# Optimization experiments

Measured on AMD Instinct MI355X. Metric: run time of the kernel, lower is better.

## Reference

```python
import jax, jax.numpy as jnp
import numpy as np

B, L, H, C = 2, 512, 128, 25

def setup_inputs() -> dict:
    key = jax.random.key(0)
    k1, k2, k3, k4 = jax.random.split(key, 4)
    x1 = jax.random.normal(k1, (B, L, H), dtype=jnp.float32)
    x2 = jax.random.normal(k2, (B, L, H), dtype=jnp.float32)
    W = jax.random.normal(k3, (C, 4 * H), dtype=jnp.float32) * (1.0 / np.sqrt(4 * H))
    b = jax.random.normal(k4, (C,), dtype=jnp.float32) * 0.01
    return {"x1": x1, "x2": x2, "W": W, "b": b}

def reference(x1, x2, W, b):
    # feat = cat([x1_i, x2_j, x1_i*x2_j, |x1_i - x2_j|]) over all (i, j) pairs,
    # then Linear(4H -> C). Split W into its 4 H-sized blocks so we never
    # materialize the [B, L, L, 4H] concatenated tensor.
    Hd = x1.shape[-1]
    W1, W2, W3, W4 = (W[:, 0:Hd], W[:, Hd:2*Hd], W[:, 2*Hd:3*Hd], W[:, 3*Hd:4*Hd])
    a = x1[:, :, None, :]   # [B, L, 1, H] -> row token
    c = x2[:, None, :, :]   # [B, 1, L, H] -> col token
    # a@W1 and c@W2 depend on only one index, so compute [B, L, C] then broadcast.
    t1 = jnp.einsum('blh,ch->blc', x1, W1)[:, :, None, :]  # [B, L, 1, C]
    t2 = jnp.einsum('blh,ch->blc', x2, W2)[:, None, :, :]  # [B, 1, L, C]
    # product term is a bilinear contraction; no [B,L,L,H] materialization needed.
    t3 = jnp.einsum('blh,bmh,ch->blmc', x1, x2, W3)         # [B, L, L, C]
    # abs-diff term requires the pairwise [B, L, L, H] tensor (nonlinear in pair).
    t4 = jnp.einsum('blmh,ch->blmc', jnp.abs(a - c), W4)    # [B, L, L, C]
    return t1 + t2 + t3 + t4 + b  # [B, L, L, C]
```

## Files before the change

kernel.cpp:

```cpp
#include <hip/hip_runtime.h>
#include <hip/hip_bf16.h>
#include <math.h>

#define BB 2
#define LL 512
#define HH 128
#define CC 25
#define W4H (4*HH)

typedef __attribute__((ext_vector_type(4))) float    f32x4;
typedef __attribute__((ext_vector_type(8))) _Float16 half8;
typedef __attribute__((ext_vector_type(2))) _Float16 half2t;
typedef __attribute__((ext_vector_type(4))) unsigned uint4v;

#define MTILE 64
#define LPB   8
#define XPH   136

static __device__ __forceinline__ half8 habs8(half8 x) {
    uint4v u = __builtin_bit_cast(uint4v, x);
    u &= 0x7FFF7FFFu;
    return __builtin_bit_cast(half8, u);
}
static __device__ __forceinline__ half2t pkrtz(float a, float b) {
    return __builtin_bit_cast(half2t, __builtin_amdgcn_cvt_pkrtz(a, b));
}
union H4 { half2t h2[2]; unsigned long long u64; };
union H8 { half2t h2[4]; uint4v u4; half8 h8; };

static __device__ __forceinline__ half8 loadWfrag(const float* __restrict__ W,
                                                  int c, int col0) {
    H8 h; h.u4 = (uint4v){0u, 0u, 0u, 0u};
    if (c < CC) {
        const float* p = W + (size_t)c * W4H + col0;
        const f32x4 v0 = *(const f32x4*)(p);
        const f32x4 v1 = *(const f32x4*)(p + 4);
        h.h2[0] = pkrtz(v0[0], v0[1]);
        h.h2[1] = pkrtz(v0[2], v0[3]);
        h.h2[2] = pkrtz(v1[0], v1[1]);
        h.h2[3] = pkrtz(v1[2], v1[3]);
    }
    return h.h8;
}

__global__ __launch_bounds__(256)
void biaffine_fused(const float* __restrict__ x1, const float* __restrict__ x2,
                    const float* __restrict__ W, const float* __restrict__ bias,
                    float* __restrict__ out)
{
    __shared__ __align__(16) _Float16 x1h[LPB * XPH];
    __shared__ __align__(16) float    t1s[LPB * 32];

    const int tid = threadIdx.x;
    const int b   = blockIdx.z;
    const int l0  = blockIdx.y * LPB;
    const int m0  = blockIdx.x * MTILE;

    const int lane = tid & 63;
    const int wv   = tid >> 6;
    const int q    = lane >> 4;
    const int cn   = lane & 15;

    {
        const float* sx1 = x1 + ((size_t)b * LL + l0) * HH;
        const int r  = tid >> 5;
        const int c4 = tid & 31;
        const f32x4 v = *(const f32x4*)(sx1 + r * HH + c4 * 4);
        H4 h;
        h.h2[0] = pkrtz(v[0], v[1]);
        h.h2[1] = pkrtz(v[2], v[3]);
        *(unsigned long long*)(&x1h[r * XPH + c4 * 4]) = h.u64;
    }
    __syncthreads();

    const int mrowA = wv * 16 + cn;
    half8 X2f[4];
    {
        const float* px2 = x2 + ((size_t)b * LL + m0 + mrowA) * HH;
        #pragma unroll
        for (int hh = 0; hh < 4; ++hh) {
            const float* p = px2 + hh * 32 + q * 8;
            const f32x4 v0 = *(const f32x4*)(p);
            const f32x4 v1 = *(const f32x4*)(p + 4);
            H8 h;
            h.h2[0] = pkrtz(v0[0], v0[1]);
            h.h2[1] = pkrtz(v0[2], v0[3]);
            h.h2[2] = pkrtz(v1[0], v1[1]);
            h.h2[3] = pkrtz(v1[2], v1[3]);
            X2f[hh] = h.h8;
        }
    }

    f32x4 t2a = {0.f,0.f,0.f,0.f}, t2b = {0.f,0.f,0.f,0.f};
    #pragma unroll
    for (int kk = 0; kk < 4; ++kk) {
        const int col0 = HH + kk * 32 + q * 8;
        const half8 b0 = loadWfrag(W, cn,      col0);
        const half8 b1 = loadWfrag(W, cn + 16, col0);
        t2a = __builtin_amdgcn_mfma_f32_16x16x32_f16(X2f[kk], b0, t2a, 0, 0, 0);
        t2b = __builtin_amdgcn_mfma_f32_16x16x32_f16(X2f[kk], b1, t2b, 0, 0, 0);
    }

    if (wv == 0) {
        f32x4 t1acc0 = {0.f,0.f,0.f,0.f}, t1acc1 = {0.f,0.f,0.f,0.f};
        #pragma unroll
        for (int kk = 0; kk < 4; ++kk) {
            const half8 a1 = *(const half8*)(&x1h[(cn & 7) * XPH + kk * 32 + q * 8]);
            const int col0 = kk * 32 + q * 8;
            const half8 b0 = loadWfrag(W, cn,      col0);
            const half8 b1 = loadWfrag(W, cn + 16, col0);
            t1acc0 = __builtin_amdgcn_mfma_f32_16x16x32_f16(a1, b0, t1acc0, 0, 0, 0);
            t1acc1 = __builtin_amdgcn_mfma_f32_16x16x32_f16(a1, b1, t1acc1, 0, 0, 0);
        }
        if (q < 2) {
            const float ba = bias[cn];
            const float bb = (cn + 16 < CC) ? bias[cn + 16] : 0.f;
            #pragma unroll
            for (int r = 0; r < 4; ++r) {
                const int l = q * 4 + r;
                t1s[l * 32 + cn]      = t1acc0[r] + ba;
                t1s[l * 32 + 16 + cn] = t1acc1[r] + bb;
            }
        }
    }

    half8 Bf0[8], Bf1[8];
    #pragma unroll
    for (int kk = 0; kk < 8; ++kk) {
        const int col0 = 2 * HH + kk * 32 + q * 8;
        Bf0[kk] = loadWfrag(W, cn,      col0);
        Bf1[kk] = loadWfrag(W, cn + 16, col0);
    }
    __syncthreads();

    const bool cok = (cn + 16 < CC);

    #pragma unroll
    for (int l = 0; l < LPB; ++l) {
        f32x4 acc0 = {0.f,0.f,0.f,0.f};
        f32x4 acc1 = {0.f,0.f,0.f,0.f};

        #pragma unroll
        for (int hh = 0; hh < 4; ++hh) {
            const half8 a  = *(const half8*)(&x1h[l * XPH + hh * 32 + q * 8]);
            const half8 bq = X2f[hh];
            const half8 Ap = a * bq;
            const half8 Ad = habs8(a - bq);
            acc0 = __builtin_amdgcn_mfma_f32_16x16x32_f16(Ap, Bf0[hh],     acc0, 0, 0, 0);
            acc1 = __builtin_amdgcn_mfma_f32_16x16x32_f16(Ap, Bf1[hh],     acc1, 0, 0, 0);
            acc0 = __builtin_amdgcn_mfma_f32_16x16x32_f16(Ad, Bf0[4 + hh], acc0, 0, 0, 0);
            acc1 = __builtin_amdgcn_mfma_f32_16x16x32_f16(Ad, Bf1[4 + hh], acc1, 0, 0, 0);
        }

        const int lg = l0 + l;
        const float t1a = t1s[l * 32 + cn];
        const float t1b = t1s[l * 32 + 16 + cn];
        float* obase = out + (((size_t)b * LL + lg) * LL + (m0 + wv * 16 + q * 4)) * CC + cn;
        #pragma unroll
        for (int r = 0; r < 4; ++r) {
            obase[(size_t)r * CC] = acc0[r] + t1a + t2a[r];
            if (cok) obase[(size_t)r * CC + 16] = acc1[r] + t1b + t2b[r];
        }
    }
}

extern "C" void kernel_launch(void* const* d_in, const int* in_sizes, int n_in,
                              void* d_out, int out_size, void* d_ws, size_t ws_size,
                              hipStream_t stream) {
    const float* x1   = (const float*)d_in[0];
    const float* x2   = (const float*)d_in[1];
    const float* W    = (const float*)d_in[2];
    const float* bias = (const float*)d_in[3];
    float* out = (float*)d_out;

    dim3 grid(LL / MTILE, LL / LPB, BB);
    biaffine_fused<<<grid, 256, 0, stream>>>(x1, x2, W, bias, out);
}
```

Before: 105.1 us.

## Pre-pack W fragments and x1/x2 to fp16 in a separate pack kernel

Adds a small pre-pass kernel that converts W into MFMA-ready fp16 fragments laid out per lane, and converts x1/x2 to fp16 in workspace. The main kernel then loads the packed halves directly instead of having every block reload fp32 W and run the conversions. This cuts redundant global traffic and conversion ALU work per block. In exchange it adds a second launch and a dependency on workspace, and it drops the LDS row padding for x1, which may bring back bank conflicts.

After: 90.23 us. 1.16x faster.

```diff
diff --git a/kernel.cpp b/kernel.cpp
--- a/kernel.cpp
+++ b/kernel.cpp
@@ -15,7 +15,10 @@
 
 #define MTILE 64
 #define LPB   8
-#define XPH   136
+
+#define NFRAG 2048
+#define WS_X_OFF (NFRAG*8)
+#define XELS (BB*LL*HH)
 
 static __device__ __forceinline__ half8 habs8(half8 x) {
     uint4v u = __builtin_bit_cast(uint4v, x);
@@ -28,27 +31,55 @@
 union H4 { half2t h2[2]; unsigned long long u64; };
 union H8 { half2t h2[4]; uint4v u4; half8 h8; };
 
-static __device__ __forceinline__ half8 loadWfrag(const float* __restrict__ W,
-                                                  int c, int col0) {
-    H8 h; h.u4 = (uint4v){0u, 0u, 0u, 0u};
-    if (c < CC) {
-        const float* p = W + (size_t)c * W4H + col0;
-        const f32x4 v0 = *(const f32x4*)(p);
-        const f32x4 v1 = *(const f32x4*)(p + 4);
+__global__ __launch_bounds__(256)
+void pack_kernel(const float* __restrict__ x1, const float* __restrict__ x2,
+                 const float* __restrict__ W, _Float16* __restrict__ ws)
+{
+    const int gid = blockIdx.x * 256 + threadIdx.x;
+
+    if (gid < NFRAG) {
+        const int ln  = gid & 63;
+        const int t   = (gid >> 6) & 1;
+        const int kk  = gid >> 7;
+        const int c   = (ln & 15) + 16 * t;
+        const int k0  = kk * 32 + ((ln >> 4) << 3);
+        const int wc  = (k0 + 256) & 511;
+        H8 h; h.u4 = (uint4v){0u, 0u, 0u, 0u};
+        if (c < CC) {
+            const float* p = W + (size_t)c * W4H + wc;
+            const f32x4 v0 = *(const f32x4*)(p);
+            const f32x4 v1 = *(const f32x4*)(p + 4);
+            h.h2[0] = pkrtz(v0[0], v0[1]);
+            h.h2[1] = pkrtz(v0[2], v0[3]);
+            h.h2[2] = pkrtz(v1[0], v1[1]);
+            h.h2[3] = pkrtz(v1[2], v1[3]);
+        }
+        *(uint4v*)(ws + (size_t)gid * 8) = h.u4;
+    }
+
+    _Float16* wsX = ws + WS_X_OFF;
+    #pragma unroll
+    for (int i = 0; i < 8; ++i) {
+        const int ch  = gid + i * 4096;
+        const int arr = ch >> 14;
+        const int off = (ch & 16383) * 8;
+        const float* src = (arr ? x2 : x1) + off;
+        const f32x4 v0 = *(const f32x4*)(src);
+        const f32x4 v1 = *(const f32x4*)(src + 4);
+        H8 h;
         h.h2[0] = pkrtz(v0[0], v0[1]);
         h.h2[1] = pkrtz(v0[2], v0[3]);
         h.h2[2] = pkrtz(v1[0], v1[1]);
         h.h2[3] = pkrtz(v1[2], v1[3]);
+        *(uint4v*)(wsX + (size_t)ch * 8) = h.u4;
     }
-    return h.h8;
 }
 
 __global__ __launch_bounds__(256)
-void biaffine_fused(const float* __restrict__ x1, const float* __restrict__ x2,
-                    const float* __restrict__ W, const float* __restrict__ bias,
+void biaffine_fused(const _Float16* __restrict__ ws, const float* __restrict__ bias,
                     float* __restrict__ out)
 {
-    __shared__ __align__(16) _Float16 x1h[LPB * XPH];
+    __shared__ __align__(16) _Float16 x1h[LPB * HH];
     __shared__ __align__(16) float    t1s[LPB * 32];
 
     const int tid = threadIdx.x;
@@ -61,42 +92,34 @@
     const int q    = lane >> 4;
     const int cn   = lane & 15;
 
-    {
-        const float* sx1 = x1 + ((size_t)b * LL + l0) * HH;
-        const int r  = tid >> 5;
-        const int c4 = tid & 31;
-        const f32x4 v = *(const f32x4*)(sx1 + r * HH + c4 * 4);
-        H4 h;
-        h.h2[0] = pkrtz(v[0], v[1]);
-        h.h2[1] = pkrtz(v[2], v[3]);
-        *(unsigned long long*)(&x1h[r * XPH + c4 * 4]) = h.u64;
-    }
+    const _Float16* wsWf = ws;
+    const _Float16* x1p  = ws + WS_X_OFF;
+    const _Float16* x2p  = x1p + XELS;
+
+    if (tid < 128)
+        *(uint4v*)(&x1h[tid * 8]) =
+            *(const uint4v*)(x1p + ((size_t)b * LL + l0) * HH + tid * 8);
     __syncthreads();
 
     const int mrowA = wv * 16 + cn;
+    const _Float16* px2 = x2p + ((size_t)b * LL + m0 + mrowA) * HH;
     half8 X2f[4];
-    {
-        const float* px2 = x2 + ((size_t)b * LL + m0 + mrowA) * HH;
-        #pragma unroll
-        for (int hh = 0; hh < 4; ++hh) {
-            const float* p = px2 + hh * 32 + q * 8;
-            const f32x4 v0 = *(const f32x4*)(p);
-            const f32x4 v1 = *(const f32x4*)(p + 4);
-            H8 h;
-            h.h2[0] = pkrtz(v0[0], v0[1]);
-            h.h2[1] = pkrtz(v0[2], v0[3]);
-            h.h2[2] = pkrtz(v1[0], v1[1]);
-            h.h2[3] = pkrtz(v1[2], v1[3]);
-            X2f[hh] = h.h8;
-        }
+    #pragma unroll
+    for (int hh = 0; hh < 4; ++hh)
+        X2f[hh] = *(const half8*)(px2 + hh * 32 + q * 8);
+
+    half8 Bf0[8], Bf1[8];
+    #pragma unroll
+    for (int kk = 0; kk < 8; ++kk) {
+        Bf0[kk] = *(const half8*)(wsWf + ((size_t)(kk * 2 + 0) * 64 + lane) * 8);
+        Bf1[kk] = *(const half8*)(wsWf + ((size_t)(kk * 2 + 1) * 64 + lane) * 8);
     }
 
     f32x4 t2a = {0.f,0.f,0.f,0.f}, t2b = {0.f,0.f,0.f,0.f};
     #pragma unroll
     for (int kk = 0; kk < 4; ++kk) {
-        const int col0 = HH + kk * 32 + q * 8;
-        const half8 b0 = loadWfrag(W, cn,      col0);
-        const half8 b1 = loadWfrag(W, cn + 16, col0);
+        const half8 b0 = *(const half8*)(wsWf + ((size_t)((12 + kk) * 2 + 0) * 64 + lane) * 8);
+        const half8 b1 = *(const half8*)(wsWf + ((size_t)((12 + kk) * 2 + 1) * 64 + lane) * 8);
         t2a = __builtin_amdgcn_mfma_f32_16x16x32_f16(X2f[kk], b0, t2a, 0, 0, 0);
         t2b = __builtin_amdgcn_mfma_f32_16x16x32_f16(X2f[kk], b1, t2b, 0, 0, 0);
     }
@@ -105,10 +128,9 @@
         f32x4 t1acc0 = {0.f,0.f,0.f,0.f}, t1acc1 = {0.f,0.f,0.f,0.f};
         #pragma unroll
         for (int kk = 0; kk < 4; ++kk) {
-            const half8 a1 = *(const half8*)(&x1h[(cn & 7) * XPH + kk * 32 + q * 8]);
-            const int col0 = kk * 32 + q * 8;
-            const half8 b0 = loadWfrag(W, cn,      col0);
-            const half8 b1 = loadWfrag(W, cn + 16, col0);
+            const half8 a1 = *(const half8*)(&x1h[(cn & 7) * HH + kk * 32 + q * 8]);
+            const half8 b0 = *(const half8*)(wsWf + ((size_t)((8 + kk) * 2 + 0) * 64 + lane) * 8);
+            const half8 b1 = *(const half8*)(wsWf + ((size_t)((8 + kk) * 2 + 1) * 64 + lane) * 8);
             t1acc0 = __builtin_amdgcn_mfma_f32_16x16x32_f16(a1, b0, t1acc0, 0, 0, 0);
             t1acc1 = __builtin_amdgcn_mfma_f32_16x16x32_f16(a1, b1, t1acc1, 0, 0, 0);
         }
@@ -123,14 +145,6 @@
             }
         }
     }
-
-    half8 Bf0[8], Bf1[8];
-    #pragma unroll
-    for (int kk = 0; kk < 8; ++kk) {
-        const int col0 = 2 * HH + kk * 32 + q * 8;
-        Bf0[kk] = loadWfrag(W, cn,      col0);
-        Bf1[kk] = loadWfrag(W, cn + 16, col0);
-    }
     __syncthreads();
 
     const bool cok = (cn + 16 < CC);
@@ -142,7 +156,7 @@
 
         #pragma unroll
         for (int hh = 0; hh < 4; ++hh) {
-            const half8 a  = *(const half8*)(&x1h[l * XPH + hh * 32 + q * 8]);
+            const half8 a  = *(const half8*)(&x1h[l * HH + hh * 32 + q * 8]);
             const half8 bq = X2f[hh];
             const half8 Ap = a * bq;
             const half8 Ad = habs8(a - bq);
@@ -172,7 +186,10 @@
     const float* W    = (const float*)d_in[2];
     const float* bias = (const float*)d_in[3];
     float* out = (float*)d_out;
+    _Float16* ws = (_Float16*)d_ws;
+
+    pack_kernel<<<16, 256, 0, stream>>>(x1, x2, W, ws);
 
     dim3 grid(LL / MTILE, LL / LPB, BB);
-    biaffine_fused<<<grid, 256, 0, stream>>>(x1, x2, W, bias, out);
+    biaffine_fused<<<grid, 256, 0, stream>>>(ws, bias, out);
 }
```
